# Kernel optimization log

Measured on AMD Instinct MI355X. Metric: run time of the kernel, lower is better.

Reference implementation:

```python
import jax, jax.numpy as jnp
import numpy as np

B, N, L, H, D, IN = 512, 128, 10, 16, 8, 16
NT = B * N
E = NT * 16

def _lin(key, fan_in, shape):
    b = 1.0 / np.sqrt(fan_in)
    return jax.random.uniform(key, shape, jnp.float32, -b, b)

def setup_inputs() -> dict:
    key = jax.random.key(0)
    ks = jax.random.split(key, 12)
    x = jax.random.normal(ks[0], (NT, IN), jnp.float32)
    # within-graph random edges so to_dense_adj is well defined
    g = jax.random.randint(ks[1], (E,), 0, B)
    i = jax.random.randint(ks[2], (E,), 0, N)
    j = jax.random.randint(ks[3], (E,), 0, N)
    edge_index = jnp.stack([g * N + i, g * N + j]).astype(jnp.int32)
    return dict(
        x=x,
        gin_w1=_lin(ks[4], H, (2, L, H, H)),   # [ld/ud, layer, H, H]
        gin_b1=_lin(ks[5], H, (2, L, H)),
        gin_w2=_lin(ks[6], H, (2, L, H, H)),
        gin_b2=_lin(ks[7], H, (2, L, H)),
        mean_w=_lin(ks[8], H, (2, H, D)),
        mean_b=jnp.zeros((2, D), jnp.float32),
        std_w=_lin(ks[9], H, (2, H, D)),
        std_b=jnp.zeros((2, D), jnp.float32),
        edge_index=edge_index,
    )

def _encoder(x, w1, b1, w2, b2, mw, mb, sw, sb, src, dst):
    # PyG GIN stack: GINConv(MLP[Lin->ReLU->Lin]), eps=0, sum aggregation,
    # ReLU between layers (dropout = identity in eval mode).
    h = x
    for l in range(L):
        agg = jax.ops.segment_sum(h[src], dst, num_segments=NT)
        t = h + agg  # (1+eps)*x + sum_{j in N(i)} x_j with eps=0
        t = jnp.maximum(t @ w1[l] + b1[l], 0.0) @ w2[l] + b2[l]
        h = jnp.maximum(t, 0.0) if l < L - 1 else t
    mean = h @ mw + mb
    std = jax.nn.softplus(h @ sw + sb)
    return mean, std

def reference(x, gin_w1, gin_b1, gin_w2, gin_b2, mean_w, mean_b, std_w, std_b, edge_index):
    src, dst = edge_index[0], edge_index[1]
    enc = jax.vmap(_encoder, in_axes=(None, 0, 0, 0, 0, 0, 0, 0, 0, None, None))
    mean, std = enc(x, gin_w1, gin_b1, gin_w2, gin_b2,
                    mean_w, mean_b, std_w, std_b, src, dst)  # [2, NT, D]
    # reparameterized sample: eps ~ N(0,1) (prior.sample, detached)
    eps = jax.random.normal(jax.random.key(42), (2, NT, D), jnp.float32)
    z = mean + std * eps
    z_ld = z[0].reshape(B, N, D)
    z_ud = z[1].reshape(B, N, D)
    logits = jnp.einsum('bnd,bmd->bnm', z_ld, z_ud)  # per-graph inner-product decode
    dense_adj = jnp.zeros((B, N, N), jnp.float32).at[src // N, src % N, dst % N].add(1.0)
    n_pos = dense_adj.sum()
    posw = (B * N * N - n_pos) / n_pos
    # BCE-with-logits, pos_weight, reduction='sum'
    nll = jnp.sum(posw * dense_adj * jax.nn.softplus(-logits)
                  + (1.0 - dense_adj) * jax.nn.softplus(logits))
    # KL(N(mean,std) || N(0,1)), summed over both encoders
    kl = jnp.sum(-jnp.log(std) + 0.5 * (std * std + mean * mean) - 0.5)
    return nll, kl, jax.nn.sigmoid(logits), dense_adj
```

## Files before the change

### kernel.cpp

```cpp
#include <hip/hip_runtime.h>

#define B_    512
#define N_    128
#define L_    10
#define H_    16
#define D_    8
#define NT_   65536
#define E_    1048576
#define NNB_  8388608
#define CAP_  4096
#define CCAP_ 2816
#define HS_   20

__device__ __forceinline__ unsigned rotl32(unsigned v, int r){ return (v<<r)|(v>>(32-r)); }

__device__ __forceinline__ void threefry2x32(unsigned c0, unsigned c1, unsigned &o0, unsigned &o1){
  const unsigned ks0 = 0u, ks1 = 42u, ks2 = 0u ^ 42u ^ 0x1BD11BDAu;
  unsigned x0 = c0 + ks0, x1 = c1 + ks1;
#define TFR(r) { x0 += x1; x1 = rotl32(x1, r); x1 ^= x0; }
  TFR(13) TFR(15) TFR(26) TFR(6)   x0 += ks1; x1 += ks2 + 1u;
  TFR(17) TFR(29) TFR(16) TFR(24)  x0 += ks2; x1 += ks0 + 2u;
  TFR(13) TFR(15) TFR(26) TFR(6)   x0 += ks0; x1 += ks1 + 3u;
  TFR(17) TFR(29) TFR(16) TFR(24)  x0 += ks1; x1 += ks2 + 4u;
  TFR(13) TFR(15) TFR(26) TFR(6)   x0 += ks2; x1 += ks0 + 5u;
#undef TFR
  o0 = x0; o1 = x1;
}

__device__ __forceinline__ float erfinv_f(float x){
  float w = -log1pf(-x*x);
  float p;
  if (w < 5.0f) {
    w -= 2.5f;
    p = 2.81022636e-08f;
    p = fmaf(p, w, 3.43273939e-07f);
    p = fmaf(p, w, -3.5233877e-06f);
    p = fmaf(p, w, -4.39150654e-06f);
    p = fmaf(p, w, 0.00021858087f);
    p = fmaf(p, w, -0.00125372503f);
    p = fmaf(p, w, -0.00417768164f);
    p = fmaf(p, w, 0.246640727f);
    p = fmaf(p, w, 1.50140941f);
  } else {
    w = sqrtf(w) - 3.0f;
    p = -0.000200214257f;
    p = fmaf(p, w, 0.000100950558f);
    p = fmaf(p, w, 0.00134934322f);
    p = fmaf(p, w, -0.00367342844f);
    p = fmaf(p, w, 0.00573950773f);
    p = fmaf(p, w, -0.0076224613f);
    p = fmaf(p, w, 0.00943887047f);
    p = fmaf(p, w, 1.00167406f);
    p = fmaf(p, w, 2.83297682f);
  }
  return p * x;
}

__device__ __forceinline__ float softplus_f(float x){
  return fmaxf(x, 0.0f) + log1pf(expf(-fabsf(x)));
}

__device__ __forceinline__ void blockReduceAdd(double v, double* target){
  __shared__ double red[8];
  int lane = threadIdx.x & 63;
  int w    = threadIdx.x >> 6;
  #pragma unroll
  for(int off = 32; off > 0; off >>= 1) v += __shfl_down(v, off);
  if(lane == 0) red[w] = v;
  __syncthreads();
  if(threadIdx.x == 0){
    double s = red[0];
    int nw = (blockDim.x + 63) >> 6;
    for(int k = 1; k < nw; k++) s += red[k];
    atomicAdd(target, s);
  }
}

__global__ __launch_bounds__(256)
void k_bin(const int* __restrict__ ei, int* __restrict__ gcount,
           unsigned short* __restrict__ ebuf){
  __shared__ int cnt[512];
  __shared__ int gb[512];
  const int t = threadIdx.x;
  cnt[t] = 0; cnt[t + 256] = 0;
  __syncthreads();
  int kv[8];
  const int base = blockIdx.x * 2048;
  #pragma unroll
  for(int q = 0; q < 8; q++){
    int e = base + q*256 + t;
    int s = ei[e];
    int d = ei[E_ + e];
    int g = d >> 7;
    kv[q] = (g << 14) | ((s & 127) << 7) | (d & 127);
    atomicAdd(&cnt[g], 1);
  }
  __syncthreads();
  #pragma unroll
  for(int g = 0; g < 512; g += 256){
    int c = cnt[g + t];
    gb[g + t] = c ? atomicAdd(&gcount[g + t], c) : 0;
    cnt[g + t] = 0;
  }
  __syncthreads();
  #pragma unroll
  for(int q = 0; q < 8; q++){
    int g = kv[q] >> 14;
    int pos = atomicAdd(&cnt[g], 1);
    int idx = gb[g] + pos;
    if(idx < CAP_) ebuf[(size_t)g*CAP_ + idx] = (unsigned short)(kv[q] & 0x3FFF);
  }
}

__global__ __launch_bounds__(512, 8)
void k_mega(const float* __restrict__ x, const unsigned short* __restrict__ ebuf,
            const int* __restrict__ gcount,
            const float* __restrict__ gw1, const float* __restrict__ gb1,
            const float* __restrict__ gw2, const float* __restrict__ gb2,
            const float* __restrict__ mw,  const float* __restrict__ mb,
            const float* __restrict__ sw,  const float* __restrict__ sb,
            float* __restrict__ z, double* acc){
  __shared__ __align__(16) float hh[129*HS_ + 4];
  __shared__ __align__(16) float agg_l[128*HS_];
  __shared__ __align__(16) float u_l[128*HS_];
  __shared__ __align__(16) unsigned short col_l[CCAP_];
  __shared__ int cnt[128];
  __shared__ int sc[128];
  __shared__ int off_l[129];

  const int b = blockIdx.x, e = blockIdx.y, t = threadIdx.x;
  const int lane = t & 63;
  const int q  = __builtin_amdgcn_readfirstlane((t >> 6) & 3);
  const int q4 = q * 4;
  const int n  = lane + ((t >> 8) << 6);

  {
    const float4* x4 = (const float4*)x + (size_t)b*512;
    float4 v = x4[t];
    *(float4*)&hh[(t >> 2)*HS_ + (t & 3)*4] = v;
    if(t < 16) hh[128*HS_ + t] = 0.0f;
    if(t < 128) cnt[t] = 0;
  }
  __syncthreads();

  int ec = gcount[b]; if(ec > CAP_) ec = CAP_;
  const unsigned short* eb = ebuf + (size_t)b*CAP_;
  for(int i = t; i < ec; i += 512) atomicAdd(&cnt[eb[i] & 127], 1);
  __syncthreads();
  int pdeg = 0;
  if(t < 128){ pdeg = (cnt[t] + 3) & ~3; sc[t] = pdeg; }
  __syncthreads();
  for(int o = 1; o < 128; o <<= 1){
    int v = 0;
    if(t < 128 && t >= o) v = sc[t - o];
    __syncthreads();
    if(t < 128) sc[t] += v;
    __syncthreads();
  }
  if(t < 128){ off_l[t] = sc[t] - pdeg; cnt[t] = 0; }
  if(t == 127) off_l[128] = sc[127];
  {
    uint4 s128; s128.x = s128.y = s128.z = s128.w = 0x00800080u;
    uint4* c4 = (uint4*)col_l;
    if(t < CCAP_/8) c4[t] = s128;
  }
  __syncthreads();
  for(int i = t; i < ec; i += 512){
    int pk = eb[i];
    int d = pk & 127;
    int pos = atomicAdd(&cnt[d], 1);
    int idx = off_l[d] + pos;
    if(idx < CCAP_) col_l[idx] = (unsigned short)(pk >> 7);
  }
  __syncthreads();
  const int r0 = off_l[n], r1 = off_l[n + 1];

  const float* w1g = gw1 + e*(L_*256);
  const float* w2g = gw2 + e*(L_*256);
  const float* b1g = gb1 + e*(L_*16);
  const float* b2g = gb2 + e*(L_*16);

  for(int l = 0; l < L_; l++){
    float ag0, ag1, ag2, ag3;
    {
      float4 s = *(const float4*)&hh[n*HS_ + q4];
      ag0 = s.x; ag1 = s.y; ag2 = s.z; ag3 = s.w;
    }
    for(int r = r0; r < r1; r += 4){
      ushort4 c4 = *(const ushort4*)&col_l[r];
      float4 v0 = *(const float4*)&hh[c4.x*HS_ + q4];
      float4 v1 = *(const float4*)&hh[c4.y*HS_ + q4];
      float4 v2 = *(const float4*)&hh[c4.z*HS_ + q4];
      float4 v3 = *(const float4*)&hh[c4.w*HS_ + q4];
      ag0 += v0.x + v1.x + v2.x + v3.x;
      ag1 += v0.y + v1.y + v2.y + v3.y;
      ag2 += v0.z + v1.z + v2.z + v3.z;
      ag3 += v0.w + v1.w + v2.w + v3.w;
    }
    *(float4*)&agg_l[n*HS_ + q4] = make_float4(ag0, ag1, ag2, ag3);
    __syncthreads();

    float av[16];
    {
      const float4* ap = (const float4*)&agg_l[n*HS_];
      float4 a0 = ap[0], a1 = ap[1], a2 = ap[2], a3 = ap[3];
      av[0]=a0.x; av[1]=a0.y; av[2]=a0.z; av[3]=a0.w;
      av[4]=a1.x; av[5]=a1.y; av[6]=a1.z; av[7]=a1.w;
      av[8]=a2.x; av[9]=a2.y; av[10]=a2.z; av[11]=a2.w;
      av[12]=a3.x; av[13]=a3.y; av[14]=a3.z; av[15]=a3.w;
    }
    const float* w1c = w1g + l*256 + q4;
    float u0 = b1g[l*16 + q4 + 0];
    float u1 = b1g[l*16 + q4 + 1];
    float u2 = b1g[l*16 + q4 + 2];
    float u3 = b1g[l*16 + q4 + 3];
    #pragma unroll
    for(int k = 0; k < 16; k++){
      float a = av[k];
      const float* wr = w1c + k*16;
      u0 = fmaf(a, wr[0], u0);
      u1 = fmaf(a, wr[1], u1);
      u2 = fmaf(a, wr[2], u2);
      u3 = fmaf(a, wr[3], u3);
    }
    u0 = fmaxf(u0, 0.0f); u1 = fmaxf(u1, 0.0f);
    u2 = fmaxf(u2, 0.0f); u3 = fmaxf(u3, 0.0f);
    *(float4*)&u_l[n*HS_ + q4] = make_float4(u0, u1, u2, u3);
    __syncthreads();

    float uv[16];
    {
      const float4* up = (const float4*)&u_l[n*HS_];
      float4 a0 = up[0], a1 = up[1], a2 = up[2], a3 = up[3];
      uv[0]=a0.x; uv[1]=a0.y; uv[2]=a0.z; uv[3]=a0.w;
      uv[4]=a1.x; uv[5]=a1.y; uv[6]=a1.z; uv[7]=a1.w;
      uv[8]=a2.x; uv[9]=a2.y; uv[10]=a2.z; uv[11]=a2.w;
      uv[12]=a3.x; uv[13]=a3.y; uv[14]=a3.z; uv[15]=a3.w;
    }
    const float* w2c = w2g + l*256 + q4;
    float o0 = b2g[l*16 + q4 + 0];
    float o1 = b2g[l*16 + q4 + 1];
    float o2 = b2g[l*16 + q4 + 2];
    float o3 = b2g[l*16 + q4 + 3];
    #pragma unroll
    for(int k = 0; k < 16; k++){
      float a = uv[k];
      const float* wr = w2c + k*16;
      o0 = fmaf(a, wr[0], o0);
      o1 = fmaf(a, wr[1], o1);
      o2 = fmaf(a, wr[2], o2);
      o3 = fmaf(a, wr[3], o3);
    }
    if(l < L_ - 1){
      o0 = fmaxf(o0, 0.0f); o1 = fmaxf(o1, 0.0f);
      o2 = fmaxf(o2, 0.0f); o3 = fmaxf(o3, 0.0f);
    }
    *(float4*)&hh[n*HS_ + q4] = make_float4(o0, o1, o2, o3);
    __syncthreads();
  }

  float hv[16];
  {
    const float4* hp = (const float4*)&hh[n*HS_];
    float4 a0 = hp[0], a1 = hp[1], a2 = hp[2], a3 = hp[3];
    hv[0]=a0.x; hv[1]=a0.y; hv[2]=a0.z; hv[3]=a0.w;
    hv[4]=a1.x; hv[5]=a1.y; hv[6]=a1.z; hv[7]=a1.w;
    hv[8]=a2.x; hv[9]=a2.y; hv[10]=a2.z; hv[11]=a2.w;
    hv[12]=a3.x; hv[13]=a3.y; hv[14]=a3.z; hv[15]=a3.w;
  }
  const float* mwg = mw + e*128; const float* mbg = mb + e*8;
  const float* swg = sw + e*128; const float* sbg = sb + e*8;
  double kll = 0.0;
  float zv[2];
  unsigned nodeBase = ((unsigned)e*NT_ + (unsigned)(b*128 + n))*8u;
  #pragma unroll
  for(int dd = 0; dd < 2; dd++){
    int d = q*2 + dd;
    float mm = mbg[d], ss = sbg[d];
    #pragma unroll
    for(int k = 0; k < 16; k++){
      mm = fmaf(hv[k], mwg[k*8 + d], mm);
      ss = fmaf(hv[k], swg[k*8 + d], ss);
    }
    float stdv = softplus_f(ss);
    unsigned o0, o1; threefry2x32(0u, nodeBase + (unsigned)d, o0, o1);
    unsigned bits = o0 ^ o1;
    float uu = __uint_as_float((bits >> 9) | 0x3f800000u) - 1.0f;
    const float lo = -0.99999994f;
    float uval = fmaxf(lo, fmaf(uu, 2.0f, lo));
    float eps = 1.41421356f * erfinv_f(uval);
    zv[dd] = mm + stdv * eps;
    float stdc = fmaxf(stdv, 1e-37f);
    float term = 0.5f*(stdv*stdv + mm*mm) - logf(stdc) - 0.5f;
    if(!(term == term) || term > 1e30f) term = 1e30f;
    kll += (double)term;
  }
  *(float2*)&z[nodeBase + (unsigned)(q*2)] = make_float2(zv[0], zv[1]);
  blockReduceAdd(kll, acc + 1);
}

#define TSB_ 132
__global__ __launch_bounds__(256, 4)
void k_decode(const float* __restrict__ z, const unsigned short* __restrict__ ebuf,
              const int* __restrict__ gcount, float* __restrict__ sig,
              float* __restrict__ adj, double* acc){
  __shared__ float zl[1024];
  __shared__ float zu[1152];
  __shared__ unsigned tile32[128*TSB_/4];
  const int b = blockIdx.x, t = threadIdx.x;
  const float* zld = z + (size_t)b*1024;
  const float* zud = z + (size_t)NT_*8 + (size_t)b*1024;
  for(int k = t; k < 1024; k += 256){
    zl[k] = zld[k];
    zu[(k >> 3)*9 + (k & 7)] = zud[k];
  }
  {
    uint4 zz; zz.x = zz.y = zz.z = zz.w = 0u;
    uint4* t4 = (uint4*)tile32;
    for(int k = t; k < 128*TSB_/16; k += 256) t4[k] = zz;
  }
  __syncthreads();
  {
    int ec = gcount[b]; if(ec > CAP_) ec = CAP_;
    const unsigned short* eb = ebuf + (size_t)b*CAP_;
    for(int q = t; q < ec; q += 256){
      int pk = eb[q];
      int cell = (pk >> 7)*TSB_ + (pk & 127);
      atomicAdd(&tile32[cell >> 2], 1u << ((cell & 3)*8));
    }
  }
  __syncthreads();
  double local = 0.0;
  float* sigb = sig + (size_t)b*16384;
  float* adjb = adj + (size_t)b*16384;
  for(int it = 0; it < 16; it++){
    int base = it*1024 + t*4;
    int n = base >> 7, mcol = base & 127;
    const float* za = &zl[n*8];
    float xs[4];
    #pragma unroll
    for(int c = 0; c < 4; c++){
      const float* zb = &zu[(mcol + c)*9];
      float xx = 0.0f;
      #pragma unroll
      for(int d = 0; d < 8; d++) xx = fmaf(za[d], zb[d], xx);
      xs[c] = xx;
    }
    unsigned packed = tile32[(n*TSB_ + mcol) >> 2];
    float4 av;
    av.x = (float)( packed        & 0xFF);
    av.y = (float)((packed >> 8)  & 0xFF);
    av.z = (float)((packed >> 16) & 0xFF);
    av.w = (float)((packed >> 24) & 0xFF);
    float ads[4] = {av.x, av.y, av.z, av.w};
    float sgs[4];
    #pragma unroll
    for(int c = 0; c < 4; c++){
      float xx = xs[c];
      sgs[c] = 1.0f / (1.0f + expf(-xx));
      float cc  = log1pf(expf(-fabsf(xx)));
      float spp = fmaxf(xx, 0.0f) + cc;
      float spn = fmaxf(-xx, 0.0f) + cc;
      local += (double)(7.0f*ads[c]*spn + (1.0f - ads[c])*spp);
    }
    ((float4*)(sigb + base))[0] = make_float4(sgs[0], sgs[1], sgs[2], sgs[3]);
    ((float4*)(adjb + base))[0] = av;
  }
  blockReduceAdd(local, acc + 0);
}

__device__ __forceinline__ float clamp_finite(double v){
  if(v != v) return 0.0f;
  if(v >  3.3e38) return  3.3e38f;
  if(v < -3.3e38) return -3.3e38f;
  return (float)v;
}
__global__ void k_final(const double* __restrict__ acc, float* __restrict__ out){
  if(threadIdx.x == 0){
    out[0] = clamp_finite(acc[0]);
    out[1] = clamp_finite(acc[1]);
  }
}

extern "C" void kernel_launch(void* const* d_in, const int* in_sizes, int n_in,
                              void* d_out, int out_size, void* d_ws, size_t ws_size,
                              hipStream_t stream){
  const float* x   = (const float*)d_in[0];
  const float* gw1 = (const float*)d_in[1];
  const float* gb1 = (const float*)d_in[2];
  const float* gw2 = (const float*)d_in[3];
  const float* gb2 = (const float*)d_in[4];
  const float* mw  = (const float*)d_in[5];
  const float* mb  = (const float*)d_in[6];
  const float* sw  = (const float*)d_in[7];
  const float* sb  = (const float*)d_in[8];
  const int*   ei  = (const int*)d_in[9];

  float* out = (float*)d_out;
  float* sig = out + 2;
  float* adj = out + 2 + NNB_;

  char* ws = (char*)d_ws;
  int*            gcount = (int*)(ws);
  double*         acc    = (double*)(ws + 2048);
  unsigned short* ebuf   = (unsigned short*)(ws + 4096);
  float*          z      = (float*)(ws + 4096 + 2*512*CAP_);

  hipMemsetAsync(ws, 0, 4096, stream);

  k_bin   <<<E_/2048, 256, 0, stream>>>(ei, gcount, ebuf);
  k_mega  <<<dim3(B_, 2), 512, 0, stream>>>(x, ebuf, gcount, gw1, gb1, gw2, gb2,
                                            mw, mb, sw, sb, z, acc);
  k_decode<<<B_, 256, 0, stream>>>(z, ebuf, gcount, sig, adj, acc);
  k_final <<<1, 64, 0, stream>>>(acc, out);
}
```

Measured before the change: 233.6 us.

## Merge both encoders into one 1024-thread block and split decode rows across blocks

k_mega now runs both encoders (ld/ud) in a single 1024-thread block per graph, so the edge CSR build (degree count, scan, column fill) is done once and shared instead of twice. The block-level prefix scan is replaced by a single-wave shuffle scan, and the aliasing of cnt onto hh removes some shared arrays. k_decode is split into 4 row-chunks per graph with a smaller shared tile, and it now accumulates in float per iteration before converting to double. In exchange, each k_mega block uses twice the shared memory and threads, and each decode block rescans all edges of its graph.

```diff
diff --git a/kernel.cpp b/kernel.cpp
--- a/kernel.cpp
+++ b/kernel.cpp
@@ -11,6 +11,7 @@
 #define CAP_  4096
 #define CCAP_ 2816
 #define HS_   20
+#define PLANE_ (129*HS_ + 4)
 
 __device__ __forceinline__ unsigned rotl32(unsigned v, int r){ return (v<<r)|(v>>(32-r)); }
 
@@ -61,7 +62,7 @@
 }
 
 __device__ __forceinline__ void blockReduceAdd(double v, double* target){
-  __shared__ double red[8];
+  __shared__ double red[16];
   int lane = threadIdx.x & 63;
   int w    = threadIdx.x >> 6;
   #pragma unroll
@@ -112,7 +113,7 @@
   }
 }
 
-__global__ __launch_bounds__(512, 8)
+__global__ __launch_bounds__(1024, 8)
 void k_mega(const float* __restrict__ x, const unsigned short* __restrict__ ebuf,
             const int* __restrict__ gcount,
             const float* __restrict__ gw1, const float* __restrict__ gb1,
@@ -120,52 +121,53 @@
             const float* __restrict__ mw,  const float* __restrict__ mb,
             const float* __restrict__ sw,  const float* __restrict__ sb,
             float* __restrict__ z, double* acc){
-  __shared__ __align__(16) float hh[129*HS_ + 4];
-  __shared__ __align__(16) float agg_l[128*HS_];
-  __shared__ __align__(16) float u_l[128*HS_];
+  __shared__ __align__(16) float hh[2*PLANE_];
+  __shared__ __align__(16) float agg_l[2*128*HS_];
+  __shared__ __align__(16) float u_l[2*128*HS_];
   __shared__ __align__(16) unsigned short col_l[CCAP_];
-  __shared__ int cnt[128];
-  __shared__ int sc[128];
   __shared__ int off_l[129];
 
-  const int b = blockIdx.x, e = blockIdx.y, t = threadIdx.x;
-  const int lane = t & 63;
-  const int q  = __builtin_amdgcn_readfirstlane((t >> 6) & 3);
+  const int b = blockIdx.x, t = threadIdx.x;
+  const int n  = t & 127;
+  const int q  = __builtin_amdgcn_readfirstlane((t >> 7) & 3);
+  const int e  = __builtin_amdgcn_readfirstlane(t >> 9);
   const int q4 = q * 4;
-  const int n  = lane + ((t >> 8) << 6);
-
-  {
-    const float4* x4 = (const float4*)x + (size_t)b*512;
-    float4 v = x4[t];
-    *(float4*)&hh[(t >> 2)*HS_ + (t & 3)*4] = v;
-    if(t < 16) hh[128*HS_ + t] = 0.0f;
-    if(t < 128) cnt[t] = 0;
-  }
-  __syncthreads();
-
-  int ec = gcount[b]; if(ec > CAP_) ec = CAP_;
-  const unsigned short* eb = ebuf + (size_t)b*CAP_;
-  for(int i = t; i < ec; i += 512) atomicAdd(&cnt[eb[i] & 127], 1);
-  __syncthreads();
-  int pdeg = 0;
-  if(t < 128){ pdeg = (cnt[t] + 3) & ~3; sc[t] = pdeg; }
-  __syncthreads();
-  for(int o = 1; o < 128; o <<= 1){
-    int v = 0;
-    if(t < 128 && t >= o) v = sc[t - o];
-    __syncthreads();
-    if(t < 128) sc[t] += v;
-    __syncthreads();
-  }
-  if(t < 128){ off_l[t] = sc[t] - pdeg; cnt[t] = 0; }
-  if(t == 127) off_l[128] = sc[127];
+
+  int* cnt = (int*)hh;
+
+  if(t < 128) cnt[t] = 0;
   {
     uint4 s128; s128.x = s128.y = s128.z = s128.w = 0x00800080u;
     uint4* c4 = (uint4*)col_l;
     if(t < CCAP_/8) c4[t] = s128;
   }
   __syncthreads();
-  for(int i = t; i < ec; i += 512){
+
+  int ec = gcount[b]; if(ec > CAP_) ec = CAP_;
+  const unsigned short* eb = ebuf + (size_t)b*CAP_;
+  for(int i = t; i < ec; i += 1024) atomicAdd(&cnt[eb[i] & 127], 1);
+  __syncthreads();
+
+  if(t < 64){
+    int lane = t;
+    int a0 = (cnt[lane]      + 3) & ~3;
+    int a1 = (cnt[64 + lane] + 3) & ~3;
+    int s0 = a0, s1 = a1;
+    #pragma unroll
+    for(int o = 1; o < 64; o <<= 1){
+      int v0 = __shfl_up(s0, o);
+      int v1 = __shfl_up(s1, o);
+      if(lane >= o){ s0 += v0; s1 += v1; }
+    }
+    int totA = __shfl(s0, 63);
+    off_l[lane]      = s0 - a0;
+    off_l[64 + lane] = totA + s1 - a1;
+    if(lane == 63) off_l[128] = totA + s1;
+    cnt[lane] = 0; cnt[64 + lane] = 0;
+  }
+  __syncthreads();
+
+  for(int i = t; i < ec; i += 1024){
     int pk = eb[i];
     int d = pk & 127;
     int pos = atomicAdd(&cnt[d], 1);
@@ -175,6 +177,19 @@
   __syncthreads();
   const int r0 = off_l[n], r1 = off_l[n + 1];
 
+  if(t < 512){
+    const float4* x4 = (const float4*)x + (size_t)b*512;
+    float4 v = x4[t];
+    int row = t >> 2, c = (t & 3)*4;
+    *(float4*)&hh[row*HS_ + c]          = v;
+    *(float4*)&hh[PLANE_ + row*HS_ + c] = v;
+  }
+  if(t < 16){ hh[128*HS_ + t] = 0.0f; hh[PLANE_ + 128*HS_ + t] = 0.0f; }
+  __syncthreads();
+
+  const float* hb   = hh    + e*PLANE_;
+  float*       aggb = agg_l + e*(128*HS_);
+  float*       ub   = u_l   + e*(128*HS_);
   const float* w1g = gw1 + e*(L_*256);
   const float* w2g = gw2 + e*(L_*256);
   const float* b1g = gb1 + e*(L_*16);
@@ -183,26 +198,26 @@
   for(int l = 0; l < L_; l++){
     float ag0, ag1, ag2, ag3;
     {
-      float4 s = *(const float4*)&hh[n*HS_ + q4];
+      float4 s = *(const float4*)&hb[n*HS_ + q4];
       ag0 = s.x; ag1 = s.y; ag2 = s.z; ag3 = s.w;
     }
     for(int r = r0; r < r1; r += 4){
       ushort4 c4 = *(const ushort4*)&col_l[r];
-      float4 v0 = *(const float4*)&hh[c4.x*HS_ + q4];
-      float4 v1 = *(const float4*)&hh[c4.y*HS_ + q4];
-      float4 v2 = *(const float4*)&hh[c4.z*HS_ + q4];
-      float4 v3 = *(const float4*)&hh[c4.w*HS_ + q4];
+      float4 v0 = *(const float4*)&hb[c4.x*HS_ + q4];
+      float4 v1 = *(const float4*)&hb[c4.y*HS_ + q4];
+      float4 v2 = *(const float4*)&hb[c4.z*HS_ + q4];
+      float4 v3 = *(const float4*)&hb[c4.w*HS_ + q4];
       ag0 += v0.x + v1.x + v2.x + v3.x;
       ag1 += v0.y + v1.y + v2.y + v3.y;
       ag2 += v0.z + v1.z + v2.z + v3.z;
       ag3 += v0.w + v1.w + v2.w + v3.w;
     }
-    *(float4*)&agg_l[n*HS_ + q4] = make_float4(ag0, ag1, ag2, ag3);
+    *(float4*)&aggb[n*HS_ + q4] = make_float4(ag0, ag1, ag2, ag3);
     __syncthreads();
 
     float av[16];
     {
-      const float4* ap = (const float4*)&agg_l[n*HS_];
+      const float4* ap = (const float4*)&aggb[n*HS_];
       float4 a0 = ap[0], a1 = ap[1], a2 = ap[2], a3 = ap[3];
       av[0]=a0.x; av[1]=a0.y; av[2]=a0.z; av[3]=a0.w;
       av[4]=a1.x; av[5]=a1.y; av[6]=a1.z; av[7]=a1.w;
@@ -225,12 +240,12 @@
     }
     u0 = fmaxf(u0, 0.0f); u1 = fmaxf(u1, 0.0f);
     u2 = fmaxf(u2, 0.0f); u3 = fmaxf(u3, 0.0f);
-    *(float4*)&u_l[n*HS_ + q4] = make_float4(u0, u1, u2, u3);
+    *(float4*)&ub[n*HS_ + q4] = make_float4(u0, u1, u2, u3);
     __syncthreads();
 
     float uv[16];
     {
-      const float4* up = (const float4*)&u_l[n*HS_];
+      const float4* up = (const float4*)&ub[n*HS_];
       float4 a0 = up[0], a1 = up[1], a2 = up[2], a3 = up[3];
       uv[0]=a0.x; uv[1]=a0.y; uv[2]=a0.z; uv[3]=a0.w;
       uv[4]=a1.x; uv[5]=a1.y; uv[6]=a1.z; uv[7]=a1.w;
@@ -255,13 +270,13 @@
       o0 = fmaxf(o0, 0.0f); o1 = fmaxf(o1, 0.0f);
       o2 = fmaxf(o2, 0.0f); o3 = fmaxf(o3, 0.0f);
     }
-    *(float4*)&hh[n*HS_ + q4] = make_float4(o0, o1, o2, o3);
+    *(float4*)&hh[e*PLANE_ + n*HS_ + q4] = make_float4(o0, o1, o2, o3);
     __syncthreads();
   }
 
   float hv[16];
   {
-    const float4* hp = (const float4*)&hh[n*HS_];
+    const float4* hp = (const float4*)&hb[n*HS_];
     float4 a0 = hp[0], a1 = hp[1], a2 = hp[2], a3 = hp[3];
     hv[0]=a0.x; hv[1]=a0.y; hv[2]=a0.z; hv[3]=a0.w;
     hv[4]=a1.x; hv[5]=a1.y; hv[6]=a1.z; hv[7]=a1.w;
@@ -300,40 +315,38 @@
 }
 
 #define TSB_ 132
-__global__ __launch_bounds__(256, 4)
+__global__ __launch_bounds__(256, 8)
 void k_decode(const float* __restrict__ z, const unsigned short* __restrict__ ebuf,
               const int* __restrict__ gcount, float* __restrict__ sig,
               float* __restrict__ adj, double* acc){
-  __shared__ float zl[1024];
+  __shared__ float zl[256];
   __shared__ float zu[1152];
-  __shared__ unsigned tile32[128*TSB_/4];
-  const int b = blockIdx.x, t = threadIdx.x;
-  const float* zld = z + (size_t)b*1024;
+  __shared__ unsigned tile32[32*TSB_/4];
+  const int b = blockIdx.x, cy = blockIdx.y, t = threadIdx.x;
+  const int row0 = cy * 32;
+  const float* zld = z + (size_t)b*1024 + (size_t)row0*8;
   const float* zud = z + (size_t)NT_*8 + (size_t)b*1024;
-  for(int k = t; k < 1024; k += 256){
-    zl[k] = zld[k];
-    zu[(k >> 3)*9 + (k & 7)] = zud[k];
-  }
-  {
-    uint4 zz; zz.x = zz.y = zz.z = zz.w = 0u;
-    uint4* t4 = (uint4*)tile32;
-    for(int k = t; k < 128*TSB_/16; k += 256) t4[k] = zz;
-  }
+  for(int k = t; k < 1024; k += 256) zu[(k >> 3)*9 + (k & 7)] = zud[k];
+  zl[t] = zld[t];
+  for(int k = t; k < 32*TSB_/4; k += 256) tile32[k] = 0u;
   __syncthreads();
   {
     int ec = gcount[b]; if(ec > CAP_) ec = CAP_;
     const unsigned short* eb = ebuf + (size_t)b*CAP_;
-    for(int q = t; q < ec; q += 256){
-      int pk = eb[q];
-      int cell = (pk >> 7)*TSB_ + (pk & 127);
-      atomicAdd(&tile32[cell >> 2], 1u << ((cell & 3)*8));
+    for(int qq = t; qq < ec; qq += 256){
+      int pk = eb[qq];
+      int r = (pk >> 7) - row0;
+      if((unsigned)r < 32u){
+        int cell = r*TSB_ + (pk & 127);
+        atomicAdd(&tile32[cell >> 2], 1u << ((cell & 3)*8));
+      }
     }
   }
   __syncthreads();
   double local = 0.0;
-  float* sigb = sig + (size_t)b*16384;
-  float* adjb = adj + (size_t)b*16384;
-  for(int it = 0; it < 16; it++){
+  float* sigb = sig + (size_t)b*16384 + (size_t)row0*128;
+  float* adjb = adj + (size_t)b*16384 + (size_t)row0*128;
+  for(int it = 0; it < 4; it++){
     int base = it*1024 + t*4;
     int n = base >> 7, mcol = base & 127;
     const float* za = &zl[n*8];
@@ -354,6 +367,7 @@
     av.w = (float)((packed >> 24) & 0xFF);
     float ads[4] = {av.x, av.y, av.z, av.w};
     float sgs[4];
+    float fl = 0.0f;
     #pragma unroll
     for(int c = 0; c < 4; c++){
       float xx = xs[c];
@@ -361,8 +375,9 @@
       float cc  = log1pf(expf(-fabsf(xx)));
       float spp = fmaxf(xx, 0.0f) + cc;
       float spn = fmaxf(-xx, 0.0f) + cc;
-      local += (double)(7.0f*ads[c]*spn + (1.0f - ads[c])*spp);
-    }
+      fl += 7.0f*ads[c]*spn + (1.0f - ads[c])*spp;
+    }
+    local += (double)fl;
     ((float4*)(sigb + base))[0] = make_float4(sgs[0], sgs[1], sgs[2], sgs[3]);
     ((float4*)(adjb + base))[0] = av;
   }
@@ -409,8 +424,8 @@
   hipMemsetAsync(ws, 0, 4096, stream);
 
   k_bin   <<<E_/2048, 256, 0, stream>>>(ei, gcount, ebuf);
-  k_mega  <<<dim3(B_, 2), 512, 0, stream>>>(x, ebuf, gcount, gw1, gb1, gw2, gb2,
-                                            mw, mb, sw, sb, z, acc);
-  k_decode<<<B_, 256, 0, stream>>>(z, ebuf, gcount, sig, adj, acc);
+  k_mega  <<<B_, 1024, 0, stream>>>(x, ebuf, gcount, gw1, gb1, gw2, gb2,
+                                    mw, mb, sw, sb, z, acc);
+  k_decode<<<dim3(B_, 4), 256, 0, stream>>>(z, ebuf, gcount, sig, adj, acc);
   k_final <<<1, 64, 0, stream>>>(acc, out);
 }
```

New measurement: 241.5 us. 3.4% more time.
